# Kernel tuning notes

Hardware: AMD Instinct MI355X
Metric: run time of the kernel (lower is better)

## Reference

```python
import jax, jax.numpy as jnp
import numpy as np

D_MODEL = 1024
D_K = 1024
B = 4
T = 2048

def setup_inputs() -> dict:
    key = jax.random.key(0)
    k_x, k_q, k_k, k_v = jax.random.split(key, 4)
    s = 1.0 / np.sqrt(D_MODEL)
    return {
        "x": jax.random.normal(k_x, (B, T, D_MODEL), dtype=jnp.float32),
        "Wq": jax.random.normal(k_q, (D_MODEL, D_K), dtype=jnp.float32) * s,
        "Wk": jax.random.normal(k_k, (D_MODEL, D_K), dtype=jnp.float32) * s,
        "Wv": jax.random.normal(k_v, (D_MODEL, D_K), dtype=jnp.float32) * s,
    }

def reference(x, Wq, Wk, Wv):
    # x: (B, T, d_model); Wq/Wk/Wv: (d_model, d_k)
    Q = jnp.einsum('btd,dk->btk', x, Wq)
    K = jnp.einsum('btd,dk->btk', x, Wk)
    V = jnp.einsum('btd,dk->btk', x, Wv)
    scale = 1.0 / jnp.sqrt(jnp.asarray(D_K, dtype=x.dtype))
    scores = jnp.einsum('bqk,bsk->bqs', Q, K) * scale  # (B, T, T)
    t = scores.shape[1]
    causal = jnp.triu(jnp.ones((t, t), dtype=bool), k=1)  # True above diagonal
    scores = jnp.where(causal[None, :, :], jnp.asarray(-jnp.inf, dtype=scores.dtype), scores)
    weights = jax.nn.softmax(scores, axis=-1)
    # dropout p=0.0 -> identity
    return jnp.einsum('bqs,bsk->bqk', weights, V)
```

## Files before the change

kernel.cpp:

```cpp
#include <hip/hip_runtime.h>
#include <cstdint>

typedef __attribute__((ext_vector_type(4))) float f32x4;
typedef __attribute__((ext_vector_type(8))) __bf16 bf16x8;
typedef __attribute__((ext_vector_type(8))) unsigned short u16x8;

__device__ __forceinline__ unsigned short f2bf(float f) {
    union { float f; unsigned u; } v; v.f = f;
    unsigned u = v.u + 0x7FFFu + ((v.u >> 16) & 1u);
    return (unsigned short)(u >> 16);
}
__device__ __forceinline__ float bf2f(unsigned short h) {
    union { unsigned u; float f; } v; v.u = ((unsigned)h) << 16;
    return v.f;
}

__device__ __forceinline__ void gld_lds16(const void* g, void* l) {
    auto gp = reinterpret_cast<const __attribute__((address_space(1))) unsigned int*>(
        reinterpret_cast<uintptr_t>(g));
    auto lp = reinterpret_cast<__attribute__((address_space(3))) unsigned int*>(
        reinterpret_cast<uintptr_t>(l));
    __builtin_amdgcn_global_load_lds(gp, lp, 16, 0, 0);
}

#define MFMA_BF16(a, b, c) __builtin_amdgcn_mfma_f32_16x16x32_bf16((a), (b), (c), 0, 0, 0)

template<int BF16OUT>
__device__ __forceinline__ void gemm256(
    const unsigned short* __restrict__ A, int lda,
    const unsigned short* __restrict__ B, int ldb,
    void* __restrict__ C, int ldc,
    int ktiles,
    unsigned short* lA, unsigned short* lB)
{
    const int t = threadIdx.x;
    const int l = t & 63;
    const int w = t >> 6;
    const int wm = w >> 2, wn = w & 3;

    f32x4 acc[8][4];
#pragma unroll
    for (int i = 0; i < 8; ++i)
#pragma unroll
        for (int j = 0; j < 4; ++j)
#pragma unroll
            for (int e = 0; e < 4; ++e) acc[i][j][e] = 0.f;

    auto stage = [&](const unsigned short* __restrict__ G, int ld, unsigned short* L,
                     int p, int h, int kt) {
        const int k0 = kt << 6;
#pragma unroll
        for (int i = 0; i < 2; ++i) {
            const int flat = t + (i << 9);
            const int row  = (h << 7) + (flat >> 3);
            const int sc   = (flat & 7) ^ (row & 7);
            gld_lds16(G + (size_t)row * ld + k0 + (sc << 3),
                      L + (p << 14) + (h << 13) + (flat << 3));
        }
    };

    auto rdA = [&](int p, int mf, int kk) -> bf16x8 {
        const int r = (wm << 7) + (mf << 4) + (l & 15);
        const int c = (kk << 5) + ((l >> 4) << 3);
        const int ad = (((r << 6) + c) ^ ((r & 7) << 3)) + (p << 14);
        return *(const bf16x8*)(lA + ad);
    };
    auto rdB = [&](int p, int nf, int kk) -> bf16x8 {
        const int r = (wn << 6) + (nf << 4) + (l & 15);
        const int c = (kk << 5) + ((l >> 4) << 3);
        const int ad = (((r << 6) + c) ^ ((r & 7) << 3)) + (p << 14);
        return *(const bf16x8*)(lB + ad);
    };

    const int kt1 = (ktiles > 1) ? 1 : 0;
    stage(B, ldb, lB, 0, 0, 0); stage(B, ldb, lB, 0, 1, 0);
    stage(A, lda, lA, 0, 0, 0); stage(A, lda, lA, 0, 1, 0);
    stage(B, ldb, lB, 1, 0, kt1); stage(B, ldb, lB, 1, 1, kt1);
    asm volatile("s_waitcnt vmcnt(4)" ::: "memory");
    __builtin_amdgcn_s_barrier();

#define MMA_PHASE(MF0, A00, A01, A10, A11)                                    \
    __builtin_amdgcn_s_setprio(1);                                            \
    _Pragma("unroll")                                                         \
    for (int nf = 0; nf < 4; ++nf) {                                          \
        acc[MF0][nf]     = MFMA_BF16(A00, bq[nf][0], acc[MF0][nf]);           \
        acc[MF0][nf]     = MFMA_BF16(A01, bq[nf][1], acc[MF0][nf]);           \
        acc[MF0 + 1][nf] = MFMA_BF16(A10, bq[nf][0], acc[MF0 + 1][nf]);       \
        acc[MF0 + 1][nf] = MFMA_BF16(A11, bq[nf][1], acc[MF0 + 1][nf]);       \
    }                                                                         \
    __builtin_amdgcn_s_setprio(0);

    for (int kt = 0; kt < ktiles; ++kt) {
        const int p = kt & 1;
        const int ktA = (kt + 1 < ktiles) ? kt + 1 : ktiles - 1;
        const int ktB = (kt + 2 < ktiles) ? kt + 2 : ktiles - 1;

        bf16x8 bq[4][2];
#pragma unroll
        for (int nf = 0; nf < 4; ++nf) {
            bq[nf][0] = rdB(p, nf, 0);
            bq[nf][1] = rdB(p, nf, 1);
        }
        bf16x8 a00 = rdA(p, 0, 0), a01 = rdA(p, 0, 1);
        bf16x8 a10 = rdA(p, 1, 0), a11 = rdA(p, 1, 1);
        stage(A, lda, lA, p ^ 1, 0, ktA);
        __builtin_amdgcn_s_barrier();
        MMA_PHASE(0, a00, a01, a10, a11)
        __builtin_amdgcn_s_barrier();

        a00 = rdA(p, 2, 0); a01 = rdA(p, 2, 1);
        a10 = rdA(p, 3, 0); a11 = rdA(p, 3, 1);
        stage(A, lda, lA, p ^ 1, 1, ktA);
        stage(B, ldb, lB, p, 0, ktB);
        __builtin_amdgcn_s_barrier();
        MMA_PHASE(2, a00, a01, a10, a11)
        __builtin_amdgcn_s_barrier();

        a00 = rdA(p, 4, 0); a01 = rdA(p, 4, 1);
        a10 = rdA(p, 5, 0); a11 = rdA(p, 5, 1);
        stage(B, ldb, lB, p, 1, ktB);
        __builtin_amdgcn_s_barrier();
        MMA_PHASE(4, a00, a01, a10, a11)
        __builtin_amdgcn_s_barrier();

        a00 = rdA(p, 6, 0); a01 = rdA(p, 6, 1);
        a10 = rdA(p, 7, 0); a11 = rdA(p, 7, 1);
        __builtin_amdgcn_s_barrier();
        MMA_PHASE(6, a00, a01, a10, a11)
        asm volatile("s_waitcnt vmcnt(4)" ::: "memory");
        __builtin_amdgcn_s_barrier();
    }
#undef MMA_PHASE

#pragma unroll
    for (int mf = 0; mf < 8; ++mf)
#pragma unroll
        for (int nf = 0; nf < 4; ++nf)
#pragma unroll
            for (int j = 0; j < 4; ++j) {
                const int row = (wm << 7) + (mf << 4) + ((l >> 4) << 2) + j;
                const int col = (wn << 6) + (nf << 4) + (l & 15);
                const float v = acc[mf][nf][j];
                if (BF16OUT)
                    ((unsigned short*)C)[(size_t)row * ldc + col] = f2bf(v);
                else
                    ((float*)C)[(size_t)row * ldc + col] = v;
            }
}

template<int BF16OUT>
__device__ __forceinline__ void gemm8(
    const unsigned short* __restrict__ A, int lda,
    const unsigned short* __restrict__ B, int ldb,
    void* __restrict__ C, int ldc,
    int ktiles,
    unsigned short* lA, unsigned short* lB)
{
    const int t = threadIdx.x;
    const int l = t & 63;
    const int w = t >> 6;
    const int wr = w >> 1, wc = w & 1;

    f32x4 acc[2][4];
#pragma unroll
    for (int i = 0; i < 2; ++i)
#pragma unroll
        for (int j = 0; j < 4; ++j)
#pragma unroll
            for (int e = 0; e < 4; ++e) acc[i][j][e] = 0.f;

    auto stage = [&](int p, int kt) {
        const int k0 = kt << 6;
#pragma unroll
        for (int i = 0; i < 2; ++i) {
            const int flat = t + (i << 9);
            const int row = flat >> 3;
            const int sc = (flat & 7) ^ (row & 7);
            gld_lds16(A + (size_t)row * lda + k0 + (sc << 3), lA + (p << 13) + (flat << 3));
            gld_lds16(B + (size_t)row * ldb + k0 + (sc << 3), lB + (p << 13) + (flat << 3));
        }
    };

    auto compute = [&](int p) {
#pragma unroll
        for (int kk = 0; kk < 2; ++kk) {
            bf16x8 af[2], bfr[4];
            const int c = (kk << 5) + ((l >> 4) << 3);
#pragma unroll
            for (int mf = 0; mf < 2; ++mf) {
                const int r = (wr << 5) + (mf << 4) + (l & 15);
                const int ad = (((r << 6) + c) ^ ((r & 7) << 3)) + (p << 13);
                af[mf] = *(const bf16x8*)(lA + ad);
            }
#pragma unroll
            for (int nf = 0; nf < 4; ++nf) {
                const int r = (wc << 6) + (nf << 4) + (l & 15);
                const int ad = (((r << 6) + c) ^ ((r & 7) << 3)) + (p << 13);
                bfr[nf] = *(const bf16x8*)(lB + ad);
            }
            __builtin_amdgcn_s_setprio(1);
#pragma unroll
            for (int mf = 0; mf < 2; ++mf)
#pragma unroll
                for (int nf = 0; nf < 4; ++nf)
                    acc[mf][nf] = MFMA_BF16(af[mf], bfr[nf], acc[mf][nf]);
            __builtin_amdgcn_s_setprio(0);
        }
    };

    stage(0, 0);
    __syncthreads();
    int p = 0;
    for (int kt = 0; kt < ktiles - 1; ++kt) {
        stage(p ^ 1, kt + 1);
        compute(p);
        __syncthreads();
        p ^= 1;
    }
    compute(p);

#pragma unroll
    for (int mf = 0; mf < 2; ++mf)
#pragma unroll
        for (int nf = 0; nf < 4; ++nf)
#pragma unroll
            for (int j = 0; j < 4; ++j) {
                const int row = (wr << 5) + (mf << 4) + ((l >> 4) << 2) + j;
                const int col = (wc << 6) + (nf << 4) + (l & 15);
                const float v = acc[mf][nf][j];
                if (BF16OUT)
                    ((unsigned short*)C)[(size_t)row * ldc + col] = f2bf(v);
                else
                    ((float*)C)[(size_t)row * ldc + col] = v;
            }
}

__global__ __launch_bounds__(512, 2) void k_proj256(
    const unsigned short* __restrict__ xb, const unsigned short* __restrict__ wtqk,
    const unsigned short* __restrict__ wtv,
    unsigned short* __restrict__ qk, unsigned short* __restrict__ vt)
{
    __shared__ unsigned short lA[32768], lB[32768];
    const int h = blockIdx.x;
    const int lgc = (h & 7) * 48 + (h >> 3);
    if (lgc < 256) {
        const int by = lgc >> 3, bx = lgc & 7;
        gemm256<1>(xb + (size_t)by * 256 * 1024, 1024,
                   wtqk + (size_t)bx * 256 * 1024, 1024,
                   qk + (size_t)by * 256 * 2048 + bx * 256, 2048,
                   16, lA, lB);
    } else {
        const int l2 = lgc - 256;
        const int dn = l2 & 3, tn = l2 >> 2;
        gemm256<1>(wtv + (size_t)dn * 256 * 1024, 1024,
                   xb + (size_t)tn * 256 * 1024, 1024,
                   vt + (size_t)dn * 256 * 8192 + tn * 256, 8192,
                   16, lA, lB);
    }
}

__global__ __launch_bounds__(512, 2) void k_scores256(
    const unsigned short* __restrict__ qk, unsigned short* __restrict__ S)
{
    __shared__ unsigned short lA[32768], lB[32768];
    const int b = blockIdx.z;
    const int tidx = blockIdx.x;
    int qt2 = 0;
    while ((qt2 + 1) * (qt2 + 2) / 2 <= tidx) ++qt2;
    const int kt2 = tidx - qt2 * (qt2 + 1) / 2;
    gemm256<1>(qk + ((size_t)b * 2048 + qt2 * 256) * 2048, 2048,
               qk + ((size_t)b * 2048 + kt2 * 256) * 2048 + 1024, 2048,
               S + (size_t)b * 4194304 + (size_t)qt2 * 256 * 2048 + kt2 * 256, 2048,
               16, lA, lB);
}

__global__ __launch_bounds__(512, 4) void k_pv(
    const unsigned short* __restrict__ P, const unsigned short* __restrict__ Vt,
    float* __restrict__ out)
{
    const int dn = blockIdx.x, pr = blockIdx.y, b = blockIdx.z;
    __shared__ unsigned short lA[16384], lB[16384];
    const int q1 = pr, q2 = 15 - pr;
    gemm8<0>(P + (size_t)b * 4194304 + (size_t)q1 * 128 * 2048, 2048,
             Vt + (size_t)dn * 128 * 8192 + b * 2048, 8192,
             out + ((size_t)b * 2048 + q1 * 128) * 1024 + dn * 128, 1024,
             (q1 + 1) * 2, lA, lB);
    __syncthreads();
    gemm8<0>(P + (size_t)b * 4194304 + (size_t)q2 * 128 * 2048, 2048,
             Vt + (size_t)dn * 128 * 8192 + b * 2048, 8192,
             out + ((size_t)b * 2048 + q2 * 128) * 1024 + dn * 128, 1024,
             (q2 + 1) * 2, lA, lB);
}

__global__ __launch_bounds__(256) void k_cast_bf16(
    const float* __restrict__ in, unsigned short* __restrict__ out, int n8)
{
    const int i = blockIdx.x * 256 + threadIdx.x;
    if (i >= n8) return;
    const float4* p = (const float4*)in + (size_t)i * 2;
    const float4 a = p[0], b = p[1];
    u16x8 r;
    r[0] = f2bf(a.x); r[1] = f2bf(a.y); r[2] = f2bf(a.z); r[3] = f2bf(a.w);
    r[4] = f2bf(b.x); r[5] = f2bf(b.y); r[6] = f2bf(b.z); r[7] = f2bf(b.w);
    *(u16x8*)(out + (size_t)i * 8) = r;
}

__global__ __launch_bounds__(256) void k_transpose3(
    const float* __restrict__ Wq, const float* __restrict__ Wk, const float* __restrict__ Wv,
    unsigned short* __restrict__ wtqk, unsigned short* __restrict__ wtv)
{
    __shared__ float tile[32][33];
    const int z = blockIdx.z;
    const float* in = (z == 0) ? Wq : (z == 1) ? Wk : Wv;
    unsigned short* out = (z < 2) ? (wtqk + (size_t)z * 1048576) : wtv;
    const float s = (z == 0) ? 0.03125f : 1.0f;
    const int bx = blockIdx.x * 32, by = blockIdx.y * 32;
    const int tx = threadIdx.x, ty = threadIdx.y;
    for (int r = ty; r < 32; r += 8)
        tile[r][tx] = in[(size_t)(by + r) * 1024 + bx + tx];
    __syncthreads();
    for (int r = ty; r < 32; r += 8)
        out[(size_t)(bx + r) * 1024 + by + tx] = f2bf(tile[tx][r] * s);
}

__global__ __launch_bounds__(256) void k_softmax(unsigned short* __restrict__ S)
{
    const int w = threadIdx.x >> 6, l = threadIdx.x & 63;
    const int r = blockIdx.x * 4 + w;
    const int b = r >> 11, lr = r & 2047;
    unsigned short* row = S + ((size_t)b << 22) + ((size_t)lr << 11);
    const int edge = ((lr >> 7) + 1) << 7;

    float v[32];
#pragma unroll
    for (int i = 0; i < 4; ++i) {
        const int c0 = (l << 3) + (i << 9);
        if (c0 < edge) {
            const u16x8 u = *(const u16x8*)(row + c0);
#pragma unroll
            for (int j = 0; j < 8; ++j)
                v[(i << 3) + j] = (c0 + j <= lr) ? bf2f(u[j]) : -3.0e38f;
        } else {
#pragma unroll
            for (int j = 0; j < 8; ++j) v[(i << 3) + j] = -3.0e38f;
        }
    }
    float m = v[0];
#pragma unroll
    for (int k = 1; k < 32; ++k) m = fmaxf(m, v[k]);
#pragma unroll
    for (int s = 32; s; s >>= 1) m = fmaxf(m, __shfl_xor(m, s, 64));
    float sum = 0.f;
#pragma unroll
    for (int k = 0; k < 32; ++k) { const float e = __expf(v[k] - m); v[k] = e; sum += e; }
#pragma unroll
    for (int s = 32; s; s >>= 1) sum += __shfl_xor(sum, s, 64);
    const float inv = 1.f / sum;
#pragma unroll
    for (int i = 0; i < 4; ++i) {
        const int c0 = (l << 3) + (i << 9);
        if (c0 < edge) {
            u16x8 o;
#pragma unroll
            for (int j = 0; j < 8; ++j) o[j] = f2bf(v[(i << 3) + j] * inv);
            *(u16x8*)(row + c0) = o;
        }
    }
}

extern "C" void kernel_launch(void* const* d_in, const int* in_sizes, int n_in,
                              void* d_out, int out_size, void* d_ws, size_t ws_size,
                              hipStream_t stream)
{
    (void)in_sizes; (void)n_in; (void)out_size; (void)ws_size;
    const float* x  = (const float*)d_in[0];
    const float* Wq = (const float*)d_in[1];
    const float* Wk = (const float*)d_in[2];
    const float* Wv = (const float*)d_in[3];
    float* out = (float*)d_out;

    char* w = (char*)d_ws;
    unsigned short* xb   = (unsigned short*)(w);
    unsigned short* wtqk = (unsigned short*)(w + 16777216);
    unsigned short* wtv  = (unsigned short*)(w + 20971520);
    unsigned short* QK   = (unsigned short*)(w + 23068672);
    unsigned short* Vt   = (unsigned short*)(w + 56623104);
    unsigned short* S    = (unsigned short*)(w + 73400320);

    k_cast_bf16<<<4096, 256, 0, stream>>>(x, xb, 1048576);
    k_transpose3<<<dim3(32, 32, 3), dim3(32, 8), 0, stream>>>(Wq, Wk, Wv, wtqk, wtv);

    k_proj256<<<384, 512, 0, stream>>>(xb, wtqk, wtv, QK, Vt);

    k_scores256<<<dim3(36, 1, 4), 512, 0, stream>>>(QK, S);
    k_softmax<<<2048, 256, 0, stream>>>(S);
    k_pv<<<dim3(8, 8, 4), 512, 0, stream>>>(S, Vt, out);
}
```

Baseline: 229.3 us.

## Merge prep kernels, split V projection into 128-tile GEMM, unpair PV blocks

```diff
diff --git a/kernel.cpp b/kernel.cpp
--- a/kernel.cpp
+++ b/kernel.cpp
@@ -235,28 +235,29 @@
             }
 }
 
-__global__ __launch_bounds__(512, 2) void k_proj256(
+__global__ __launch_bounds__(512, 2) void k_qk256(
     const unsigned short* __restrict__ xb, const unsigned short* __restrict__ wtqk,
-    const unsigned short* __restrict__ wtv,
-    unsigned short* __restrict__ qk, unsigned short* __restrict__ vt)
+    unsigned short* __restrict__ qk)
 {
     __shared__ unsigned short lA[32768], lB[32768];
     const int h = blockIdx.x;
-    const int lgc = (h & 7) * 48 + (h >> 3);
-    if (lgc < 256) {
-        const int by = lgc >> 3, bx = lgc & 7;
-        gemm256<1>(xb + (size_t)by * 256 * 1024, 1024,
-                   wtqk + (size_t)bx * 256 * 1024, 1024,
-                   qk + (size_t)by * 256 * 2048 + bx * 256, 2048,
-                   16, lA, lB);
-    } else {
-        const int l2 = lgc - 256;
-        const int dn = l2 & 3, tn = l2 >> 2;
-        gemm256<1>(wtv + (size_t)dn * 256 * 1024, 1024,
-                   xb + (size_t)tn * 256 * 1024, 1024,
-                   vt + (size_t)dn * 256 * 8192 + tn * 256, 8192,
-                   16, lA, lB);
-    }
+    const int lgc = (h & 7) * 32 + (h >> 3);
+    const int by = lgc >> 3, bx = lgc & 7;
+    gemm256<1>(xb + (size_t)by * 256 * 1024, 1024,
+               wtqk + (size_t)bx * 256 * 1024, 1024,
+               qk + (size_t)by * 256 * 2048 + bx * 256, 2048,
+               16, lA, lB);
+}
+
+__global__ __launch_bounds__(512, 4) void k_gemm_vt(
+    const unsigned short* __restrict__ wtv, const unsigned short* __restrict__ xb,
+    unsigned short* __restrict__ vt)
+{
+    __shared__ unsigned short lA[16384], lB[16384];
+    gemm8<1>(wtv + (size_t)blockIdx.y * 128 * 1024, 1024,
+             xb + (size_t)blockIdx.x * 128 * 1024, 1024,
+             vt + (size_t)blockIdx.y * 128 * 8192 + blockIdx.x * 128, 8192,
+             16, lA, lB);
 }
 
 __global__ __launch_bounds__(512, 2) void k_scores256(
@@ -278,44 +279,40 @@
     const unsigned short* __restrict__ P, const unsigned short* __restrict__ Vt,
     float* __restrict__ out)
 {
-    const int dn = blockIdx.x, pr = blockIdx.y, b = blockIdx.z;
+    const int dn = blockIdx.x, b = blockIdx.z;
+    const int qt = 15 - blockIdx.y;
     __shared__ unsigned short lA[16384], lB[16384];
-    const int q1 = pr, q2 = 15 - pr;
-    gemm8<0>(P + (size_t)b * 4194304 + (size_t)q1 * 128 * 2048, 2048,
+    gemm8<0>(P + (size_t)b * 4194304 + (size_t)qt * 128 * 2048, 2048,
              Vt + (size_t)dn * 128 * 8192 + b * 2048, 8192,
-             out + ((size_t)b * 2048 + q1 * 128) * 1024 + dn * 128, 1024,
-             (q1 + 1) * 2, lA, lB);
-    __syncthreads();
-    gemm8<0>(P + (size_t)b * 4194304 + (size_t)q2 * 128 * 2048, 2048,
-             Vt + (size_t)dn * 128 * 8192 + b * 2048, 8192,
-             out + ((size_t)b * 2048 + q2 * 128) * 1024 + dn * 128, 1024,
-             (q2 + 1) * 2, lA, lB);
-}
-
-__global__ __launch_bounds__(256) void k_cast_bf16(
-    const float* __restrict__ in, unsigned short* __restrict__ out, int n8)
-{
-    const int i = blockIdx.x * 256 + threadIdx.x;
-    if (i >= n8) return;
-    const float4* p = (const float4*)in + (size_t)i * 2;
-    const float4 a = p[0], b = p[1];
-    u16x8 r;
-    r[0] = f2bf(a.x); r[1] = f2bf(a.y); r[2] = f2bf(a.z); r[3] = f2bf(a.w);
-    r[4] = f2bf(b.x); r[5] = f2bf(b.y); r[6] = f2bf(b.z); r[7] = f2bf(b.w);
-    *(u16x8*)(out + (size_t)i * 8) = r;
-}
-
-__global__ __launch_bounds__(256) void k_transpose3(
+             out + ((size_t)b * 2048 + qt * 128) * 1024 + dn * 128, 1024,
+             (qt + 1) * 2, lA, lB);
+}
+
+__global__ __launch_bounds__(256) void k_prep(
+    const float* __restrict__ x,
     const float* __restrict__ Wq, const float* __restrict__ Wk, const float* __restrict__ Wv,
+    unsigned short* __restrict__ xb,
     unsigned short* __restrict__ wtqk, unsigned short* __restrict__ wtv)
 {
     __shared__ float tile[32][33];
-    const int z = blockIdx.z;
+    const int bid = blockIdx.x;
+    if (bid < 4096) {
+        const int i = bid * 256 + threadIdx.x;
+        const float4* p = (const float4*)x + (size_t)i * 2;
+        const float4 a = p[0], b = p[1];
+        u16x8 r;
+        r[0] = f2bf(a.x); r[1] = f2bf(a.y); r[2] = f2bf(a.z); r[3] = f2bf(a.w);
+        r[4] = f2bf(b.x); r[5] = f2bf(b.y); r[6] = f2bf(b.z); r[7] = f2bf(b.w);
+        *(u16x8*)(xb + (size_t)i * 8) = r;
+        return;
+    }
+    const int rbid = bid - 4096;
+    const int z = rbid >> 10, t2 = rbid & 1023;
     const float* in = (z == 0) ? Wq : (z == 1) ? Wk : Wv;
     unsigned short* out = (z < 2) ? (wtqk + (size_t)z * 1048576) : wtv;
     const float s = (z == 0) ? 0.03125f : 1.0f;
-    const int bx = blockIdx.x * 32, by = blockIdx.y * 32;
-    const int tx = threadIdx.x, ty = threadIdx.y;
+    const int bx = (t2 & 31) * 32, by = (t2 >> 5) * 32;
+    const int tx = threadIdx.x & 31, ty = threadIdx.x >> 5;
     for (int r = ty; r < 32; r += 8)
         tile[r][tx] = in[(size_t)(by + r) * 1024 + bx + tx];
     __syncthreads();
@@ -387,12 +384,12 @@
     unsigned short* Vt   = (unsigned short*)(w + 56623104);
     unsigned short* S    = (unsigned short*)(w + 73400320);
 
-    k_cast_bf16<<<4096, 256, 0, stream>>>(x, xb, 1048576);
-    k_transpose3<<<dim3(32, 32, 3), dim3(32, 8), 0, stream>>>(Wq, Wk, Wv, wtqk, wtv);
-
-    k_proj256<<<384, 512, 0, stream>>>(xb, wtqk, wtv, QK, Vt);
+    k_prep<<<7168, 256, 0, stream>>>(x, Wq, Wk, Wv, xb, wtqk, wtv);
+
+    k_qk256  <<<256, 512, 0, stream>>>(xb, wtqk, QK);
+    k_gemm_vt<<<dim3(64, 8), 512, 0, stream>>>(wtv, xb, Vt);
 
     k_scores256<<<dim3(36, 1, 4), 512, 0, stream>>>(QK, S);
     k_softmax<<<2048, 256, 0, stream>>>(S);
-    k_pv<<<dim3(8, 8, 4), 512, 0, stream>>>(S, Vt, out);
-}
+    k_pv<<<dim3(8, 16, 4), 512, 0, stream>>>(S, Vt, out);
+}
```

Result: faster. 219.1 us (-4.4%).
